# Kernel optimization log

Measured on AMD Instinct MI355X. Metric: run time of the kernel, lower is better.

## Reference

```python
import jax, jax.numpy as jnp
import numpy as np

# ---- production-scale dims ----
U, I, D = 51200, 25600, 64          # users, items, embed_size
E, EP = 1_000_000, 100_000          # train edges, pos/neg scoring edges
K = 8                               # topk similar users (FFT filter length)
NF = K // 2 + 1                     # rfft bins
CL_BS = 256                         # contrastive chunk size (U % CL_BS == 0)
TEMP = 0.2                          # args.temperature
N_LAYERS = 2                        # args.layers


def setup_inputs() -> dict:
    key = jax.random.key(0)
    ks = jax.random.split(key, 14)
    return {
        "user_emb": jax.random.normal(ks[0], (U, D), jnp.float32) * 0.1,
        "item_emb": jax.random.normal(ks[1], (I, D), jnp.float32) * 0.1,
        "W": jax.random.normal(ks[2], (D, D), jnp.float32) * (1.0 / np.sqrt(D)),
        "a": jax.random.normal(ks[3], (D,), jnp.float32) * 0.1,
        "WU": jax.random.normal(ks[4], (D, D), jnp.float32) * (1.0 / np.sqrt(D)),
        "aU": jax.random.normal(ks[5], (2 * D,), jnp.float32) * 0.1,
        "complex_weight": jax.random.normal(ks[6], (1, NF, D, 2), jnp.float32) * 0.02,
        "rate_src": jax.random.randint(ks[7], (E,), 0, U),
        "rate_dst": jax.random.randint(ks[8], (E,), 0, I),
        "pos_u": jax.random.randint(ks[9], (EP,), 0, U),
        "pos_i": jax.random.randint(ks[10], (EP,), 0, I),
        "neg_u": jax.random.randint(ks[11], (EP,), 0, U),
        "neg_i": jax.random.randint(ks[12], (EP,), 0, I),
        "nbr_idx": jax.random.randint(ks[13], (U, K), 0, U),
    }


def _propagate(src_feat, src_idx, dst_idx, n_dst):
    """DGRecLayer: degree-normalized mean aggregation over bipartite edges."""
    msg = src_feat[src_idx]                                       # [E, D] gather
    agg = jax.ops.segment_sum(msg, dst_idx, num_segments=n_dst)   # [n_dst, D] scatter
    deg = jax.ops.segment_sum(jnp.ones((src_idx.shape[0],), src_feat.dtype),
                              dst_idx, num_segments=n_dst)
    return agg / jnp.maximum(deg, 1.0)[:, None]


def _layer_attention(ls, W, a):
    t = jnp.stack(ls, axis=0)                                     # [L+1, N, D]
    alpha = jax.nn.softmax(jnp.einsum('lnd,de,e->ln', t, W, a), axis=0)
    return jnp.einsum('lnd,ln->nd', t, alpha)


def _anchor_user_embed(user_emb, WU, aU, complex_weight, nbr_idx):
    # Original detaches user embeddings to numpy for the FAISS path.
    ue = jax.lax.stop_gradient(user_emb)
    simu = ue[nbr_idx]                                            # [U, K, D]
    x = jnp.fft.rfft(simu, axis=1, norm='ortho')                  # [U, NF, D]
    wc = complex_weight[..., 0] + 1j * complex_weight[..., 1]     # [1, NF, D]
    simu = jnp.fft.irfft(x * wc, n=K, axis=1, norm='ortho')       # [U, K, D]
    Wsimu = jnp.einsum('ukd,de->uke', simu, WU)                   # [U, K, D]
    Wu = jnp.broadcast_to((ue @ WU)[:, None, :], Wsimu.shape)     # [U, K, D]
    e = jnp.concatenate([Wsimu, Wu], axis=2) @ aU                 # [U, K]
    e = jnp.where(e > 0, e, 0.1 * e)                              # LeakyReLU(0.1)
    alpha = jax.nn.softmax(e, axis=1)
    return jnp.einsum('uke,uk->ue', Wsimu, alpha)                 # [U, D]


def _chunk_contrast(r1, r2):
    B = r1.shape[0]
    n1 = jnp.linalg.norm(r1, axis=-1, keepdims=True)
    n2 = jnp.linalg.norm(r2, axis=-1, keepdims=True)
    s11 = (r1 @ r1.T) / (n1 @ n1.T + 1e-6) / TEMP
    c12 = (r1 @ r2.T) / (n1 @ n2.T + 1e-6) / TEMP
    s22 = (r2 @ r2.T) / (n2 @ n2.T + 1e-6) / TEMP
    c21 = (r2 @ r1.T) / (n2 @ n1.T + 1e-6) / TEMP
    mask = jax.nn.one_hot(jnp.arange(B), 2 * B, dtype=r1.dtype) * (-1e10)
    logits = jnp.concatenate(
        [jnp.concatenate([s11, c12], axis=-1) + mask,
         jnp.concatenate([s22, c21], axis=-1) + mask], axis=0)     # [2B, 2B]
    labels = jnp.concatenate([jnp.arange(B) + B, jnp.arange(B) + B])
    logz = jax.scipy.special.logsumexp(logits, axis=-1)
    return logz - logits[jnp.arange(2 * B), labels]                # per-example CE


def reference(user_emb, item_emb, W, a, WU, aU, complex_weight,
              rate_src, rate_dst, pos_u, pos_i, neg_u, neg_i, nbr_idx):
    h_u, h_i = user_emb, item_emb
    users, items = [h_u], [h_i]
    for _ in range(N_LAYERS):
        new_i = _propagate(h_u, rate_src, rate_dst, I)   # user -> item ('rate')
        new_u = _propagate(h_i, rate_dst, rate_src, U)   # item -> user ('rated by')
        h_u, h_i = new_u, new_i
        users.append(h_u)
        items.append(h_i)
    hu = _layer_attention(users, W, a)                   # [U, D]
    hi = _layer_attention(items, W, a)                   # [I, D]

    anchor = _anchor_user_embed(user_emb, WU, aU, complex_weight, nbr_idx)
    r1 = hu.reshape(-1, CL_BS, D)
    r2 = anchor.reshape(-1, CL_BS, D)
    loss_contrast = jax.vmap(_chunk_contrast)(r1, r2).mean()

    score_pos = jnp.sum(hu[pos_u] * hi[pos_i], axis=-1, keepdims=True)  # u_dot_v
    score_neg = jnp.sum(hu[neg_u] * hi[neg_i], axis=-1, keepdims=True)
    return score_pos, score_neg, loss_contrast
```

## Files before the change

kernel.cpp:

```cpp
#include <hip/hip_runtime.h>
#include <hip/hip_bf16.h>

constexpr int U_  = 51200;
constexpr int I_  = 25600;
constexpr int E_  = 1000000;
constexpr int EP_ = 100000;
constexpr int CB_ = 256;
constexpr int NCHUNK_ = U_ / CB_;
constexpr size_t UD_ = (size_t)U_ * 64;
constexpr size_t ID_ = (size_t)I_ * 64;
constexpr int NBK_ = 200;
constexpr int CAP_ = 8192;
constexpr int TILE_ = 4096;
constexpr int NBA_ = (E_ + TILE_ - 1) / TILE_;
constexpr int NANC_ = U_ / 16;
constexpr int NCVT_ = (int)((UD_ + ID_) / (8 * 256));

constexpr float SCALE_E_  = 16.f;
constexpr float ISCALE_E_ = 1.f / 16.f;
constexpr float SCALE_1_  = 64.f;
constexpr float ISCALE_1_ = 1.f / 64.f;

constexpr size_t OFF_LOSS  = 0;
constexpr size_t OFF_FLAG  = 1;
constexpr size_t OFF_CURU  = 8;
constexpr size_t OFF_CURI  = 208;
constexpr size_t MEMSET_BYTES = 408 * 4;
constexpr size_t OFF_VEC   = 448;
constexpr size_t OFF_BBU   = 640;
constexpr size_t OFF_BBI   = 848;
constexpr size_t OFF_ROWU  = 1088;
constexpr size_t OFF_ROWI  = ((OFF_ROWU + U_ + 1 + 63) / 64) * 64;
constexpr size_t OFF_CSRU  = ((OFF_ROWI + I_ + 1 + 63) / 64) * 64;
constexpr size_t OFF_CSRI  = OFF_CSRU + E_;
constexpr size_t OFF_U1    = ((OFF_CSRI + E_ + 63) / 64) * 64;
constexpr size_t OFF_I1    = OFF_U1 + UD_;
constexpr size_t OFF_HU    = OFF_I1 + ID_;
constexpr size_t OFF_HI    = OFF_HU + UD_;
constexpr size_t OFF_ANC   = OFF_HI + ID_;
constexpr size_t OFF_UE8   = OFF_ANC + UD_;
constexpr size_t OFF_IE8   = OFF_UE8 + UD_ / 4;
constexpr size_t OFF_U18   = OFF_IE8 + ID_ / 4;
constexpr size_t OFF_I18   = OFF_U18 + UD_ / 4;

#define DEVI static __device__ __forceinline__

typedef _Float16 h2v __attribute__((ext_vector_type(2)));
typedef _Float16 f16x8 __attribute__((ext_vector_type(8)));
typedef float floatx4 __attribute__((ext_vector_type(4)));
typedef unsigned short u16x8 __attribute__((ext_vector_type(8)));

DEVI float b2f(__hip_bfloat16 x) { return __bfloat162float(x); }

DEVI float bfb2f(unsigned short b) {
  unsigned u = ((unsigned)b) << 16; float f; __builtin_memcpy(&f, &u, 4); return f;
}

DEVI float ldf(const void* p, size_t i, int isf32) {
  if (isf32) return ((const float*)p)[i];
  return b2f(((const __hip_bfloat16*)p)[i]);
}

DEVI float frcp(float x) { return __builtin_amdgcn_rcpf(x); }

DEVI float fexp2(float x) {
#if __has_builtin(__builtin_amdgcn_exp2f)
  return __builtin_amdgcn_exp2f(x);
#else
  return exp2f(x);
#endif
}

DEVI float fp8_dec(unsigned v) {
#if __has_builtin(__builtin_amdgcn_cvt_f32_fp8)
  return __builtin_amdgcn_cvt_f32_fp8(v, 0);
#else
  unsigned b = v & 0xFF;
  if (!(b & 0x78)) return 0.f;
  unsigned short h = (unsigned short)(((b & 0x80) << 8) | (((b & 0x7f) + (8 << 3)) << 7));
  _Float16 hf; __builtin_memcpy(&hf, &h, 2);
  return (float)hf;
#endif
}

#if __has_builtin(__builtin_amdgcn_cvt_f32_fp8)
#define FP8D(w, s) __builtin_amdgcn_cvt_f32_fp8((w), (s))
#else
#define FP8D(w, s) fp8_dec(((w) >> (8 * (s))) & 0xFF)
#endif

DEVI unsigned fp8_enc_pk(float a, float b) {
#if __has_builtin(__builtin_amdgcn_cvt_pk_fp8_f32)
  return __builtin_amdgcn_cvt_pk_fp8_f32(a, b, 0u, false);
#else
  auto enc1 = [](float f) -> unsigned {
    _Float16 hf = (_Float16)f; unsigned short hb; __builtin_memcpy(&hb, &hf, 2);
    int s = hb >> 15, e = (hb >> 10) & 31, m = hb & 1023;
    int e8 = e - 15 + 7;
    int m3 = (m + ((1 << 6) + ((m >> 7) & 1))) >> 7;
    if (m3 > 7) { m3 = 0; e8++; }
    if (e8 <= 0) return (unsigned)(s << 7);
    if (e8 > 15) { e8 = 15; m3 = 6; }
    return (unsigned)((s << 7) | (e8 << 3) | m3);
  };
  return enc1(a) | (enc1(b) << 8);
#endif
}

DEVI int waveInclScan(int v, int lane) {
  #pragma unroll
  for (int off = 1; off < 64; off <<= 1) {
    int t = __shfl_up(v, off, 64);
    if (lane >= off) v += t;
  }
  return v;
}

__global__ void prep_kernel(const unsigned short* __restrict__ ueu,
                            const void* __restrict__ W, const void* __restrict__ a,
                            const void* __restrict__ WU, const void* __restrict__ aU,
                            float* __restrict__ vecs, float* __restrict__ flag) {
  int cnt = 0;
  for (int i = 0; i < 256; i++) {
    int e = (ueu[i] >> 7) & 0xFF;
    if (e >= 130) cnt++;
  }
  int isf32 = (cnt >= 8);
  if (threadIdx.x == 0) *flag = isf32 ? 1.0f : 0.0f;
  int d = threadIdx.x;
  float s = 0.f, t1 = 0.f, t2 = 0.f;
  for (int e = 0; e < 64; e++) {
    s += ldf(W, d * 64 + e, isf32) * ldf(a, e, isf32);
    float wue = ldf(WU, d * 64 + e, isf32);
    t1 += wue * ldf(aU, e, isf32);
    t2 += wue * ldf(aU, 64 + e, isf32);
  }
  vecs[d] = s;
  vecs[64 + d] = t1;
  vecs[128 + d] = t2;
}

struct BktSmem {
  int histU[NBK_], histI[NBK_];
  int loffU[NBK_ + 1], loffI[NBK_ + 1];
  int cbU[NBK_], cbI[NBK_];
  int lcU[NBK_], lcI[NBK_];
  int wsU[4], wsI[4];
  unsigned recsU[TILE_], recsI[TILE_];
};
constexpr int WS_ = 72;
struct AncSmem {
  _Float16 WUt[64 * WS_];
  _Float16 mixS[16 * WS_];
  float invSe[16];
  int nbrS[128];
};
constexpr size_t FSA_SMEM = sizeof(BktSmem) > sizeof(AncSmem) ? sizeof(BktSmem) : sizeof(AncSmem);

DEVI void bucketA_body(char* smemRaw, int blk,
    const int* __restrict__ rs, const int* __restrict__ rd,
    unsigned* __restrict__ bufU, unsigned* __restrict__ bufI,
    int* __restrict__ curU, int* __restrict__ curI) {
  BktSmem& S = *(BktSmem*)smemRaw;
  int tid = threadIdx.x;
  int base = blk * TILE_;
  for (int i = tid; i < NBK_; i += 256) { S.histU[i] = 0; S.histI[i] = 0; }
  __syncthreads();
  int ss[16], dd[16];
  #pragma unroll
  for (int t = 0; t < 16; t++) {
    int e = base + t * 256 + tid;
    bool v = e < E_;
    ss[t] = v ? rs[e] : -1;
    dd[t] = v ? rd[e] : 0;
    if (v) {
      atomicAdd(&S.histU[ss[t] >> 8], 1);
      atomicAdd(&S.histI[dd[t] >> 7], 1);
    }
  }
  __syncthreads();
  if (tid < NBK_) {
    int cU = S.histU[tid];
    S.cbU[tid] = tid * CAP_ + (cU ? atomicAdd(&curU[tid], cU) : 0);
    int cI = S.histI[tid];
    S.cbI[tid] = tid * CAP_ + (cI ? atomicAdd(&curI[tid], cI) : 0);
  }
  int lane = tid & 63, wv = tid >> 6;
  int cvU = (tid < NBK_) ? S.histU[tid] : 0;
  int cvI = (tid < NBK_) ? S.histI[tid] : 0;
  int inU = waveInclScan(cvU, lane);
  int inI = waveInclScan(cvI, lane);
  if (lane == 63) { S.wsU[wv] = inU; S.wsI[wv] = inI; }
  __syncthreads();
  int woU = 0, woI = 0;
  for (int w = 0; w < wv; w++) { woU += S.wsU[w]; woI += S.wsI[w]; }
  if (tid < NBK_) {
    S.loffU[tid] = woU + inU - cvU;
    S.loffI[tid] = woI + inI - cvI;
  }
  if (tid == NBK_ - 1) {
    S.loffU[NBK_] = woU + inU;
    S.loffI[NBK_] = woI + inI;
  }
  __syncthreads();
  if (tid < NBK_) { S.lcU[tid] = S.loffU[tid]; S.lcI[tid] = S.loffI[tid]; }
  __syncthreads();
  #pragma unroll
  for (int t = 0; t < 16; t++) {
    if (ss[t] >= 0) {
      int b = ss[t] >> 8;
      int p = atomicAdd(&S.lcU[b], 1);
      S.recsU[p] = ((unsigned)(ss[t] & 255) << 17) | (unsigned)dd[t];
      b = dd[t] >> 7;
      p = atomicAdd(&S.lcI[b], 1);
      S.recsI[p] = ((unsigned)(dd[t] & 127) << 17) | (unsigned)ss[t];
    }
  }
  __syncthreads();
  int totU = S.loffU[NBK_];
  for (int p = tid; p < totU; p += 256) {
    int lo = 0, hi = NBK_;
    while (hi - lo > 1) { int mid = (lo + hi) >> 1; if (S.loffU[mid] <= p) lo = mid; else hi = mid; }
    bufU[S.cbU[lo] + (p - S.loffU[lo])] = S.recsU[p];
  }
  int totI = S.loffI[NBK_];
  for (int p = tid; p < totI; p += 256) {
    int lo = 0, hi = NBK_;
    while (hi - lo > 1) { int mid = (lo + hi) >> 1; if (S.loffI[mid] <= p) lo = mid; else hi = mid; }
    bufI[S.cbI[lo] + (p - S.loffI[lo])] = S.recsI[p];
  }
}

DEVI void anchor_body(char* smemRaw, int blk,
    const void* __restrict__ ue, const void* __restrict__ WU,
    const void* __restrict__ cw, const float* __restrict__ vecs,
    const int* __restrict__ nbr, float* __restrict__ out, int isf32) {
  AncSmem& S = *(AncSmem*)smemRaw;
  int tid = threadIdx.x;
  int wv = tid >> 6, lane = tid & 63;
  int ublk = blk * 16;

  #pragma unroll
  for (int it = 0; it < 16; it++) {
    int k = it * 4 + wv;
    S.WUt[lane * WS_ + k] = (_Float16)ldf(WU, (size_t)k * 64 + lane, isf32);
  }
  if (tid < 128) S.nbrS[tid] = nbr[ublk * 8 + tid];
  __syncthreads();

  float cw0 = ldf(cw, (0 * 64 + lane) * 2, isf32);
  float w1r = ldf(cw, (1 * 64 + lane) * 2, isf32), w1i = ldf(cw, (1 * 64 + lane) * 2 + 1, isf32);
  float w2r = ldf(cw, (2 * 64 + lane) * 2, isf32), w2i = ldf(cw, (2 * 64 + lane) * 2 + 1, isf32);
  float w3r = ldf(cw, (3 * 64 + lane) * 2, isf32), w3i = ldf(cw, (3 * 64 + lane) * 2 + 1, isf32);
  float cw4 = ldf(cw, (4 * 64 + lane) * 2, isf32);
  float v1 = vecs[64 + lane], v2 = vecs[128 + lane];
  const float c1 = 0.70710678118654752440f;

  float xc[8], xn[8];
  #pragma unroll
  for (int k = 0; k < 8; k++)
    xc[k] = ldf(ue, (size_t)S.nbrS[wv * 32 + k] * 64 + lane, isf32);

  for (int u4 = 0; u4 < 4; u4++) {
    int uL = wv * 4 + u4;
    int u = ublk + uL;
    if (u4 < 3) {
      #pragma unroll
      for (int k = 0; k < 8; k++)
        xn[k] = ldf(ue, (size_t)S.nbrS[wv * 32 + (u4 + 1) * 8 + k] * 64 + lane, isf32);
    }
    float sA = xc[1] - xc[3] - xc[5] + xc[7];
    float sB = xc[1] + xc[3] - xc[5] - xc[7];
    float ev = (xc[0] + xc[4]) + (xc[2] + xc[6]);
    float od = (xc[1] + xc[5]) + (xc[3] + xc[7]);
    float d04 = xc[0] - xc[4], d26 = xc[2] - xc[6];
    float X0r = ev + od;
    float X1r = d04 + c1 * sA;
    float X1i = -d26 - c1 * sB;
    float X2r = (xc[0] + xc[4]) - (xc[2] + xc[6]);
    float X2i = -(xc[1] - xc[3] + xc[5] - xc[7]);
    float X3r = d04 - c1 * sA;
    float X3i = d26 - c1 * sB;
    float X4r = ev - od;
    float Zr0 = X0r * cw0;
    float Zr1 = X1r * w1r - X1i * w1i, Zi1 = X1r * w1i + X1i * w1r;
    float Zr2 = X2r * w2r - X2i * w2i, Zi2 = X2r * w2i + X2i * w2r;
    float Zr3 = X3r * w3r - X3i * w3i, Zi3 = X3r * w3i + X3i * w3r;
    float Zr4 = X4r * cw4;
    float eP = Zr0 + Zr4, eM = Zr0 - Zr4;
    float t1 = c1 * (Zr1 - Zr3), t2 = c1 * (Zi1 + Zi3);
    float y[8];
    y[0] = eP + 2.f * (Zr1 + Zr2 + Zr3);
    y[1] = eM + 2.f * (t1 - t2 - Zi2);
    y[2] = eP + 2.f * (-Zi1 - Zr2 + Zi3);
    y[3] = eM + 2.f * (-t1 - t2 + Zi2);
    y[4] = eP + 2.f * (-Zr1 + Zr2 - Zr3);
    y[5] = eM + 2.f * (-t1 + t2 - Zi2);
    y[6] = eP + 2.f * (Zi1 - Zr2 - Zi3);
    y[7] = eM + 2.f * (t1 + t2 + Zi2);
    #pragma unroll
    for (int k = 0; k < 8; k++) y[k] *= 0.125f;

    float ek[8];
    #pragma unroll
    for (int k = 0; k < 8; k++) ek[k] = y[k] * v1;
    float q = ldf(ue, (size_t)u * 64 + lane, isf32) * v2;
    #pragma unroll
    for (int off = 32; off; off >>= 1) {
      #pragma unroll
      for (int k = 0; k < 8; k++) ek[k] += __shfl_xor(ek[k], off, 64);
      q += __shfl_xor(q, off, 64);
    }
    float m = -1e30f;
    #pragma unroll
    for (int k = 0; k < 8; k++) {
      float v = ek[k] + q;
      v = v > 0.f ? v : 0.1f * v;
      ek[k] = v;
      m = fmaxf(m, v);
    }
    float se = 0.f, wexp[8];
    #pragma unroll
    for (int k = 0; k < 8; k++) { wexp[k] = __expf(ek[k] - m); se += wexp[k]; }
    float mix = 0.f;
    #pragma unroll
    for (int k = 0; k < 8; k++) mix += wexp[k] * y[k];
    S.mixS[uL * WS_ + lane] = (_Float16)mix;
    if (lane == 0) S.invSe[uL] = frcp(se);
    #pragma unroll
    for (int k = 0; k < 8; k++) xc[k] = xn[k];
  }
  __syncthreads();

  int n = lane & 15, qd = lane >> 4;
  f16x8 A0 = *(const f16x8*)&S.mixS[(lane & 15) * WS_ + qd * 8];
  f16x8 A1 = *(const f16x8*)&S.mixS[(lane & 15) * WS_ + 32 + qd * 8];
  f16x8 B0 = *(const f16x8*)&S.WUt[(wv * 16 + n) * WS_ + qd * 8];
  f16x8 B1 = *(const f16x8*)&S.WUt[(wv * 16 + n) * WS_ + 32 + qd * 8];
  const floatx4 zero = {0.f, 0.f, 0.f, 0.f};
  floatx4 acc = __builtin_amdgcn_mfma_f32_16x16x32_f16(A0, B0, zero, 0, 0, 0);
  acc = __builtin_amdgcn_mfma_f32_16x16x32_f16(A1, B1, acc, 0, 0, 0);
  #pragma unroll
  for (int r = 0; r < 4; r++) {
    int m = qd * 4 + r;
    out[(size_t)(ublk + m) * 64 + wv * 16 + n] = acc[r] * S.invSe[m];
  }
}

DEVI void convert_body(int blk, const void* __restrict__ ue, const void* __restrict__ ie,
                       unsigned char* __restrict__ ue8, unsigned char* __restrict__ ie8,
                       int isf32) {
  size_t t = (size_t)blk * 256 + threadIdx.x;
  const void* src; unsigned* dst; size_t o;
  if (t < UD_ / 8) { src = ue; dst = (unsigned*)ue8; o = t; }
  else             { src = ie; dst = (unsigned*)ie8; o = t - UD_ / 8; }
  float v[8];
  if (isf32) {
    float4 f0 = ((const float4*)src)[2 * o];
    float4 f1 = ((const float4*)src)[2 * o + 1];
    v[0] = f0.x; v[1] = f0.y; v[2] = f0.z; v[3] = f0.w;
    v[4] = f1.x; v[5] = f1.y; v[6] = f1.z; v[7] = f1.w;
  } else {
    u16x8 h = ((const u16x8*)src)[o];
    #pragma unroll
    for (int i = 0; i < 8; i++) v[i] = bfb2f(h[i]);
  }
  unsigned lo = fp8_enc_pk(v[0] * SCALE_E_, v[1] * SCALE_E_) |
                (fp8_enc_pk(v[2] * SCALE_E_, v[3] * SCALE_E_) << 16);
  unsigned hi = fp8_enc_pk(v[4] * SCALE_E_, v[5] * SCALE_E_) |
                (fp8_enc_pk(v[6] * SCALE_E_, v[7] * SCALE_E_) << 16);
  dst[2 * o]     = lo;
  dst[2 * o + 1] = hi;
}

__global__ __launch_bounds__(256) void fusedA_kernel(
    const int* __restrict__ rs, const int* __restrict__ rd,
    unsigned* __restrict__ bufU, unsigned* __restrict__ bufI,
    int* __restrict__ curU, int* __restrict__ curI,
    const void* __restrict__ ue, const void* __restrict__ ie,
    const void* __restrict__ WU, const void* __restrict__ cw,
    const float* __restrict__ vecs, const int* __restrict__ nbr,
    float* __restrict__ anc, unsigned char* __restrict__ ue8,
    unsigned char* __restrict__ ie8, const float* __restrict__ flag) {
  __shared__ __align__(16) char smem[FSA_SMEM];
  if (blockIdx.x < NBA_) {
    bucketA_body(smem, blockIdx.x, rs, rd, bufU, bufI, curU, curI);
  } else if (blockIdx.x < NBA_ + NANC_) {
    anchor_body(smem, blockIdx.x - NBA_, ue, WU, cw, vecs, nbr, anc, *flag > 0.5f);
  } else {
    convert_body(blockIdx.x - NBA_ - NANC_, ue, ie, ue8, ie8, *flag > 0.5f);
  }
}

__global__ void scanBuckets_kernel(const int* __restrict__ curU,
                                   const int* __restrict__ curI,
                                   int* __restrict__ bbU, int* __restrict__ bbI,
                                   int* __restrict__ rowU, int* __restrict__ rowI) {
  __shared__ int ws[8];
  int tid = threadIdx.x;
  int lane = tid & 63, wv = tid >> 6;
  int vU = (tid < NBK_) ? curU[tid] : 0;
  int vI = (tid < NBK_) ? curI[tid] : 0;
  int iU = waveInclScan(vU, lane);
  int iI = waveInclScan(vI, lane);
  if (lane == 63) { ws[wv] = iU; ws[4 + wv] = iI; }
  __syncthreads();
  int oU = 0, oI = 0;
  for (int w = 0; w < wv; w++) { oU += ws[w]; oI += ws[4 + w]; }
  if (tid < NBK_) { bbU[tid] = oU + iU - vU; bbI[tid] = oI + iI - vI; }
  if (tid == NBK_ - 1) { bbU[NBK_] = oU + iU; bbI[NBK_] = oI + iI; }
  if (tid == 0) { rowU[U_] = E_; rowI[I_] = E_; }
}

__global__ __launch_bounds__(256) void bucketB_kernel(
    const unsigned* __restrict__ bufU, const unsigned* __restrict__ bufI,
    const int* __restrict__ curU, const int* __restrict__ curI,
    const int* __restrict__ bbU, const int* __restrict__ bbI,
    int* __restrict__ rowU, int* __restrict__ rowI,
    int* __restrict__ csrU, int* __restrict__ csrI) {
  __shared__ int stage[CAP_];
  __shared__ int cntk[256], offk[256];
  __shared__ int wsum[4];
  int tid = threadIdx.x, b = blockIdx.x;
  int side = b >= NBK_;
  int bb = side ? b - NBK_ : b;
  const unsigned* src = (side ? bufI : bufU) + (size_t)bb * CAP_;
  int total = side ? curI[bb] : curU[bb];
  int gbase = side ? bbI[bb] : bbU[bb];
  int kpb   = side ? 128 : 256;
  int* rowptr = side ? rowI : rowU;
  int* csr    = side ? csrI : csrU;
  cntk[tid] = 0;
  __syncthreads();
  for (int r = tid; r < total; r += 256) atomicAdd(&cntk[src[r] >> 17], 1);
  __syncthreads();
  int lane = tid & 63, wv = tid >> 6;
  int cv = (tid < kpb) ? cntk[tid] : 0;
  int incl = waveInclScan(cv, lane);
  if (lane == 63) wsum[wv] = incl;
  __syncthreads();
  int wvoff = 0;
  for (int w = 0; w < wv; w++) wvoff += wsum[w];
  int excl = wvoff + incl - cv;
  if (tid < kpb) {
    offk[tid] = excl;
    rowptr[bb * kpb + tid] = gbase + excl;
  }
  __syncthreads();
  for (int r = tid; r < total; r += 256) {
    unsigned rec = src[r];
    int slot = atomicAdd(&offk[rec >> 17], 1);
    if (slot < CAP_) stage[slot] = (int)(rec & 0x1FFFFu);
  }
  __syncthreads();
  for (int s = tid; s < total; s += 256) csr[gbase + s] = stage[s];
}

__global__ __launch_bounds__(256) void agg1_kernel(
    const unsigned char* __restrict__ ue8, const unsigned char* __restrict__ ie8,
    const int* __restrict__ rowU, const int* __restrict__ rowI,
    const int* __restrict__ csrU, const int* __restrict__ csrI,
    __hip_bfloat16* __restrict__ u1, __hip_bfloat16* __restrict__ i1,
    unsigned char* __restrict__ u18, unsigned char* __restrict__ i18) {
  int wv = threadIdx.x >> 6, lane = threadIdx.x & 63;
  int sub = lane >> 4, c16 = lane & 15;
  int side = blockIdx.x >= I_ / 4;
  int blk = side ? blockIdx.x - I_ / 4 : blockIdx.x;
  int r = blk * 4 + wv;
  const int* row = side ? rowU : rowI;
  const int* csr = side ? csrU : csrI;
  const unsigned char* src = side ? ie8 : ue8;
  __hip_bfloat16* out = side ? u1 : i1;
  unsigned char* out8 = side ? u18 : i18;
  int s0 = row[r], s1 = row[r + 1];
  float a4[4] = {0.f, 0.f, 0.f, 0.f};
  int j = s0;
  for (; j + 8 <= s1; j += 8) {
    int e0 = csr[j + sub], e1 = csr[j + 4 + sub];
    unsigned w0 = *(const unsigned*)(src + (size_t)e0 * 64 + c16 * 4);
    unsigned w1 = *(const unsigned*)(src + (size_t)e1 * 64 + c16 * 4);
    a4[0] += FP8D(w0, 0) + FP8D(w1, 0);
    a4[1] += FP8D(w0, 1) + FP8D(w1, 1);
    a4[2] += FP8D(w0, 2) + FP8D(w1, 2);
    a4[3] += FP8D(w0, 3) + FP8D(w1, 3);
  }
  if (j + 4 <= s1) {
    int e0 = csr[j + sub];
    unsigned w0 = *(const unsigned*)(src + (size_t)e0 * 64 + c16 * 4);
    a4[0] += FP8D(w0, 0); a4[1] += FP8D(w0, 1);
    a4[2] += FP8D(w0, 2); a4[3] += FP8D(w0, 3);
    j += 4;
  }
  int rem = s1 - j;
  if (sub < rem) {
    int e0 = csr[j + sub];
    unsigned w0 = *(const unsigned*)(src + (size_t)e0 * 64 + c16 * 4);
    a4[0] += FP8D(w0, 0); a4[1] += FP8D(w0, 1);
    a4[2] += FP8D(w0, 2); a4[3] += FP8D(w0, 3);
  }
  #pragma unroll
  for (int c = 0; c < 4; c++) {
    a4[c] += __shfl_xor(a4[c], 16, 64);
    a4[c] += __shfl_xor(a4[c], 32, 64);
  }
  float acc = sub == 0 ? a4[0] : sub == 1 ? a4[1] : sub == 2 ? a4[2] : a4[3];
  int col = c16 * 4 + sub;
  float val = acc * ISCALE_E_ * frcp(fmaxf((float)(s1 - s0), 1.0f));
  size_t idx = (size_t)r * 64 + col;
  out[idx] = __float2bfloat16(val);
  unsigned p = fp8_enc_pk(val * SCALE_1_, val * SCALE_1_);
  out8[idx] = (unsigned char)(p & 0xFF);
}

__global__ __launch_bounds__(256) void agg2attn_kernel(
    const unsigned char* __restrict__ u18, const unsigned char* __restrict__ i18,
    const __hip_bfloat16* __restrict__ u1, const __hip_bfloat16* __restrict__ i1,
    const void* __restrict__ ue, const void* __restrict__ ie,
    const int* __restrict__ rowU, const int* __restrict__ rowI,
    const int* __restrict__ csrU, const int* __restrict__ csrI,
    const float* __restrict__ vecs, float* __restrict__ hu, float* __restrict__ hi,
    const float* __restrict__ flag) {
  int isf32 = *flag > 0.5f;
  int wv = threadIdx.x >> 6, lane = threadIdx.x & 63;
  int sub = lane >> 4, c16 = lane & 15;
  int side = blockIdx.x >= I_ / 4;
  int blk = side ? blockIdx.x - I_ / 4 : blockIdx.x;
  int r = blk * 4 + wv;
  const int* row = side ? rowU : rowI;
  const int* csr = side ? csrU : csrI;
  const unsigned char* opp8 = side ? i18 : u18;
  const __hip_bfloat16* own1 = side ? u1 : i1;
  const void* base = side ? ue : ie;
  float* h = side ? hu : hi;
  int s0 = row[r], s1 = row[r + 1];
  float a4[4] = {0.f, 0.f, 0.f, 0.f};
  int j = s0;
  for (; j + 8 <= s1; j += 8) {
    int e0 = csr[j + sub], e1 = csr[j + 4 + sub];
    unsigned w0 = *(const unsigned*)(opp8 + (size_t)e0 * 64 + c16 * 4);
    unsigned w1 = *(const unsigned*)(opp8 + (size_t)e1 * 64 + c16 * 4);
    a4[0] += FP8D(w0, 0) + FP8D(w1, 0);
    a4[1] += FP8D(w0, 1) + FP8D(w1, 1);
    a4[2] += FP8D(w0, 2) + FP8D(w1, 2);
    a4[3] += FP8D(w0, 3) + FP8D(w1, 3);
  }
  if (j + 4 <= s1) {
    int e0 = csr[j + sub];
    unsigned w0 = *(const unsigned*)(opp8 + (size_t)e0 * 64 + c16 * 4);
    a4[0] += FP8D(w0, 0); a4[1] += FP8D(w0, 1);
    a4[2] += FP8D(w0, 2); a4[3] += FP8D(w0, 3);
    j += 4;
  }
  int rem = s1 - j;
  if (sub < rem) {
    int e0 = csr[j + sub];
    unsigned w0 = *(const unsigned*)(opp8 + (size_t)e0 * 64 + c16 * 4);
    a4[0] += FP8D(w0, 0); a4[1] += FP8D(w0, 1);
    a4[2] += FP8D(w0, 2); a4[3] += FP8D(w0, 3);
  }
  #pragma unroll
  for (int c = 0; c < 4; c++) {
    a4[c] += __shfl_xor(a4[c], 16, 64);
    a4[c] += __shfl_xor(a4[c], 32, 64);
  }
  float acc = sub == 0 ? a4[0] : sub == 1 ? a4[1] : sub == 2 ? a4[2] : a4[3];
  int col = c16 * 4 + sub;
  size_t idx = (size_t)r * 64 + col;
  float t2 = acc * ISCALE_1_ * frcp(fmaxf((float)(s1 - s0), 1.0f));
  float t0 = ldf(base, idx, isf32);
  float t1 = b2f(own1[idx]);
  float w = vecs[col];
  float p0 = t0 * w, p1 = t1 * w, p2 = t2 * w;
  #pragma unroll
  for (int off = 32; off; off >>= 1) {
    p0 += __shfl_xor(p0, off, 64);
    p1 += __shfl_xor(p1, off, 64);
    p2 += __shfl_xor(p2, off, 64);
  }
  float m = fmaxf(p0, fmaxf(p1, p2));
  float e0 = __expf(p0 - m), e1 = __expf(p1 - m), e2 = __expf(p2 - m);
  float inv = 1.0f / (e0 + e1 + e2);
  h[idx] = (t0 * e0 + t1 * e1 + t2 * e2) * inv;
}

constexpr int XS_ = 72;
constexpr float SC_  = 2.6857914f;
constexpr float EPS_ = 1e-6f;
constexpr float LN2_ = 0.6931471805599453f;
__global__ __launch_bounds__(1024) void contrast_kernel(
    const float* __restrict__ hu, const float* __restrict__ an,
    float* __restrict__ loss_acc) {
  __shared__ __align__(16) _Float16 Xh[512 * XS_];
  __shared__ float iN[512];
  int tid = threadIdx.x;
  int c = blockIdx.x;

  if (tid < 512) {
    int row = tid & 255;
    const float* r1 = (tid < 256 ? hu : an) + ((size_t)c * CB_ + row) * 64;
    float4 a4[16];
    float s1 = 0.f;
    #pragma unroll
    for (int t = 0; t < 16; t++) {
      a4[t] = ((const float4*)r1)[t];
      s1 += a4[t].x * a4[t].x + a4[t].y * a4[t].y + a4[t].z * a4[t].z + a4[t].w * a4[t].w;
    }
    float inv = frcp(sqrtf(s1));
    iN[tid] = inv;
    float sc = inv * SC_;
    #pragma unroll
    for (int t = 0; t < 8; t++) {
      f16x8 v;
      v[0] = (_Float16)(a4[2*t].x * sc);   v[1] = (_Float16)(a4[2*t].y * sc);
      v[2] = (_Float16)(a4[2*t].z * sc);   v[3] = (_Float16)(a4[2*t].w * sc);
      v[4] = (_Float16)(a4[2*t+1].x * sc); v[5] = (_Float16)(a4[2*t+1].y * sc);
      v[6] = (_Float16)(a4[2*t+1].z * sc); v[7] = (_Float16)(a4[2*t+1].w * sc);
      *(f16x8*)&Xh[tid * XS_ + t * 8] = v;
    }
  }
  __syncthreads();

  int l = tid & 63, wv = tid >> 6;
  int n = l & 15, q = l >> 4;
  int rb = wv * 32;
  f16x8 A[2][2];
  #pragma unroll
  for (int t = 0; t < 2; t++) {
    A[t][0] = *(const f16x8*)&Xh[(rb + t * 16 + n) * XS_ + q * 8];
    A[t][1] = *(const f16x8*)&Xh[(rb + t * 16 + n) * XS_ + 32 + q * 8];
  }
  float eNiR[2][4];
  #pragma unroll
  for (int t = 0; t < 2; t++)
    #pragma unroll
    for (int r = 0; r < 4; r++)
      eNiR[t][r] = EPS_ * iN[rb + t * 16 + q * 4 + r];
  float sums[2][4] = {{0,0,0,0},{0,0,0,0}};
  float labs2[2] = {0, 0};
  int selfn = q * 4;
  const floatx4 zero = {0.f, 0.f, 0.f, 0.f};
  for (int ct = 0; ct < 32; ct++) {
    f16x8 B0 = *(const f16x8*)&Xh[(ct * 16 + n) * XS_ + q * 8];
    f16x8 B1 = *(const f16x8*)&Xh[(ct * 16 + n) * XS_ + 32 + q * 8];
    float iNj = iN[ct * 16 + n];
    #pragma unroll
    for (int t = 0; t < 2; t++) {
      floatx4 acc = __builtin_amdgcn_mfma_f32_16x16x32_f16(A[t][0], B0, zero, 0, 0, 0);
      acc = __builtin_amdgcn_mfma_f32_16x16x32_f16(A[t][1], B1, acc, 0, 0, 0);
      int rtg = wv * 2 + t;
      if (ct == (rtg ^ 16)) {
        #pragma unroll
        for (int r = 0; r < 4; r++) {
          float G = acc[r];
          float u = eNiR[t][r] * iNj;
          float s2 = __builtin_fmaf(G, -u, G);
          sums[t][r] += fexp2(s2);
          if (n == selfn + r) labs2[t] += s2;
        }
      } else if (ct == rtg) {
        #pragma unroll
        for (int r = 0; r < 4; r++) {
          float G = acc[r];
          float u = eNiR[t][r] * iNj;
          float s2 = __builtin_fmaf(G, -u, G);
          float e = (n == selfn + r) ? 0.f : fexp2(s2);
          sums[t][r] += e;
        }
      } else {
        #pragma unroll
        for (int r = 0; r < 4; r++) {
          float G = acc[r];
          float u = eNiR[t][r] * iNj;
          float s2 = __builtin_fmaf(G, -u, G);
          sums[t][r] += fexp2(s2);
        }
      }
    }
  }
  #pragma unroll
  for (int off = 1; off <= 8; off <<= 1) {
    #pragma unroll
    for (int t = 0; t < 2; t++) {
      #pragma unroll
      for (int r = 0; r < 4; r++) sums[t][r] += __shfl_xor(sums[t][r], off, 64);
      labs2[t] += __shfl_xor(labs2[t], off, 64);
    }
  }
  float part = 0.f;
  if (n == 0) {
    #pragma unroll
    for (int t = 0; t < 2; t++) {
      float lt = 0.f;
      #pragma unroll
      for (int r = 0; r < 4; r++) lt += __logf(sums[t][r]);
      part += lt - labs2[t] * LN2_;
    }
  }
  #pragma unroll
  for (int off = 1; off < 64; off <<= 1) part += __shfl_xor(part, off, 64);
  if (l == 0) atomicAdd(loss_acc, part);
}

__global__ __launch_bounds__(256) void score_kernel(
    const float* __restrict__ hu, const float* __restrict__ hi,
    const int* __restrict__ pu, const int* __restrict__ pi,
    const int* __restrict__ nu, const int* __restrict__ ni,
    void* __restrict__ out, const float* __restrict__ flag) {
  int isf32 = *flag > 0.5f;
  int w = (blockIdx.x * 256 + threadIdx.x) >> 6;
  int lane = threadIdx.x & 63;
  int uu, ii;
  if (w < EP_) { uu = pu[w]; ii = pi[w]; }
  else         { uu = nu[w - EP_]; ii = ni[w - EP_]; }
  float p = hu[(size_t)uu * 64 + lane] * hi[(size_t)ii * 64 + lane];
  #pragma unroll
  for (int off = 32; off; off >>= 1) p += __shfl_xor(p, off, 64);
  if (lane == 0) {
    if (isf32) ((float*)out)[w] = p;
    else       ((__hip_bfloat16*)out)[w] = __float2bfloat16(p);
  }
}

__global__ void finalize_kernel(const float* __restrict__ loss_acc,
                                void* __restrict__ out,
                                const float* __restrict__ flag) {
  float v = loss_acc[0] * (1.0f / (float)(2 * CB_ * NCHUNK_));
  if (*flag > 0.5f) ((float*)out)[2 * EP_] = v;
  else              ((__hip_bfloat16*)out)[2 * EP_] = __float2bfloat16(v);
}

extern "C" void kernel_launch(void* const* d_in, const int* in_sizes, int n_in,
                              void* d_out, int out_size, void* d_ws, size_t ws_size,
                              hipStream_t stream) {
  const void* ue  = d_in[0];
  const void* ie  = d_in[1];
  const void* W   = d_in[2];
  const void* a   = d_in[3];
  const void* WU  = d_in[4];
  const void* aU  = d_in[5];
  const void* cw  = d_in[6];
  const int* rs  = (const int*)d_in[7];
  const int* rd  = (const int*)d_in[8];
  const int* pu  = (const int*)d_in[9];
  const int* pi  = (const int*)d_in[10];
  const int* nu  = (const int*)d_in[11];
  const int* ni  = (const int*)d_in[12];
  const int* nbr = (const int*)d_in[13];

  float* wsf  = (float*)d_ws;
  int*   wsi  = (int*)d_ws;
  float* loss = wsf + OFF_LOSS;
  float* flag = wsf + OFF_FLAG;
  int* curU   = wsi + OFF_CURU;
  int* curI   = wsi + OFF_CURI;
  float* vecs = wsf + OFF_VEC;
  int* bbU    = wsi + OFF_BBU;
  int* bbI    = wsi + OFF_BBI;
  int* rowU   = wsi + OFF_ROWU;
  int* rowI   = wsi + OFF_ROWI;
  int* csrU   = wsi + OFF_CSRU;
  int* csrI   = wsi + OFF_CSRI;
  __hip_bfloat16* u1 = (__hip_bfloat16*)(wsf + OFF_U1);
  __hip_bfloat16* i1 = (__hip_bfloat16*)(wsf + OFF_I1);
  float* hu   = wsf + OFF_HU;
  float* hi   = wsf + OFF_HI;
  float* anc  = wsf + OFF_ANC;
  unsigned char* ue8 = (unsigned char*)(wsf + OFF_UE8);
  unsigned char* ie8 = (unsigned char*)(wsf + OFF_IE8);
  unsigned char* u18 = (unsigned char*)(wsf + OFF_U18);
  unsigned char* i18 = (unsigned char*)(wsf + OFF_I18);
  unsigned* bufU = (unsigned*)(wsf + OFF_HU);
  unsigned* bufI = (unsigned*)(wsf + OFF_HI);

  hipMemsetAsync(d_ws, 0, MEMSET_BYTES, stream);
  prep_kernel<<<1, 64, 0, stream>>>((const unsigned short*)ue, W, a, WU, aU, vecs, flag);

  fusedA_kernel<<<NBA_ + NANC_ + NCVT_, 256, 0, stream>>>(
      rs, rd, bufU, bufI, curU, curI, ue, ie, WU, cw, vecs, nbr, anc, ue8, ie8, flag);
  scanBuckets_kernel<<<1, 256, 0, stream>>>(curU, curI, bbU, bbI, rowU, rowI);
  bucketB_kernel<<<2 * NBK_, 256, 0, stream>>>(bufU, bufI, curU, curI, bbU, bbI,
                                               rowU, rowI, csrU, csrI);

  agg1_kernel<<<(I_ + U_) / 4, 256, 0, stream>>>(ue8, ie8, rowU, rowI, csrU, csrI,
                                                 u1, i1, u18, i18);
  agg2attn_kernel<<<(I_ + U_) / 4, 256, 0, stream>>>(u18, i18, u1, i1, ue, ie,
                                                     rowU, rowI, csrU, csrI,
                                                     vecs, hu, hi, flag);

  contrast_kernel<<<NCHUNK_, 1024, 0, stream>>>(hu, anc, loss);

  score_kernel<<<(2 * EP_ * 64) / 256, 256, 0, stream>>>(hu, hi, pu, pi, nu, ni, d_out, flag);
  finalize_kernel<<<1, 1, 0, stream>>>(loss, d_out, flag);
}
```

Measured before the change: 367.6 us.

## Fold bucket scan into bucketB, split contrast row loads, vectorize score kernel

```diff
diff --git a/kernel.cpp b/kernel.cpp
--- a/kernel.cpp
+++ b/kernel.cpp
@@ -15,6 +15,7 @@
 constexpr int NBA_ = (E_ + TILE_ - 1) / TILE_;
 constexpr int NANC_ = U_ / 16;
 constexpr int NCVT_ = (int)((UD_ + ID_) / (8 * 256));
+constexpr int NSCB_ = (2 * EP_) / 16;
 
 constexpr float SCALE_E_  = 16.f;
 constexpr float ISCALE_E_ = 1.f / 16.f;
@@ -27,8 +28,6 @@
 constexpr size_t OFF_CURI  = 208;
 constexpr size_t MEMSET_BYTES = 408 * 4;
 constexpr size_t OFF_VEC   = 448;
-constexpr size_t OFF_BBU   = 640;
-constexpr size_t OFF_BBI   = 848;
 constexpr size_t OFF_ROWU  = 1088;
 constexpr size_t OFF_ROWI  = ((OFF_ROWU + U_ + 1 + 63) / 64) * 64;
 constexpr size_t OFF_CSRU  = ((OFF_ROWI + I_ + 1 + 63) / 64) * 64;
@@ -392,68 +391,63 @@
   }
 }
 
-__global__ void scanBuckets_kernel(const int* __restrict__ curU,
-                                   const int* __restrict__ curI,
-                                   int* __restrict__ bbU, int* __restrict__ bbI,
-                                   int* __restrict__ rowU, int* __restrict__ rowI) {
-  __shared__ int ws[8];
-  int tid = threadIdx.x;
-  int lane = tid & 63, wv = tid >> 6;
-  int vU = (tid < NBK_) ? curU[tid] : 0;
-  int vI = (tid < NBK_) ? curI[tid] : 0;
-  int iU = waveInclScan(vU, lane);
-  int iI = waveInclScan(vI, lane);
-  if (lane == 63) { ws[wv] = iU; ws[4 + wv] = iI; }
-  __syncthreads();
-  int oU = 0, oI = 0;
-  for (int w = 0; w < wv; w++) { oU += ws[w]; oI += ws[4 + w]; }
-  if (tid < NBK_) { bbU[tid] = oU + iU - vU; bbI[tid] = oI + iI - vI; }
-  if (tid == NBK_ - 1) { bbU[NBK_] = oU + iU; bbI[NBK_] = oI + iI; }
-  if (tid == 0) { rowU[U_] = E_; rowI[I_] = E_; }
-}
+struct BktBSmem {
+  int stage[CAP_];
+  int cntk[256], offk[256];
+  int exclS[256];
+  int wsum[4], wsum2[4];
+};
 
 __global__ __launch_bounds__(256) void bucketB_kernel(
     const unsigned* __restrict__ bufU, const unsigned* __restrict__ bufI,
     const int* __restrict__ curU, const int* __restrict__ curI,
-    const int* __restrict__ bbU, const int* __restrict__ bbI,
     int* __restrict__ rowU, int* __restrict__ rowI,
     int* __restrict__ csrU, int* __restrict__ csrI) {
-  __shared__ int stage[CAP_];
-  __shared__ int cntk[256], offk[256];
-  __shared__ int wsum[4];
+  __shared__ __align__(16) BktBSmem S;
   int tid = threadIdx.x, b = blockIdx.x;
   int side = b >= NBK_;
   int bb = side ? b - NBK_ : b;
   const unsigned* src = (side ? bufI : bufU) + (size_t)bb * CAP_;
-  int total = side ? curI[bb] : curU[bb];
-  int gbase = side ? bbI[bb] : bbU[bb];
+  const int* cur = side ? curI : curU;
+  int total = cur[bb];
   int kpb   = side ? 128 : 256;
   int* rowptr = side ? rowI : rowU;
   int* csr    = side ? csrI : csrU;
-  cntk[tid] = 0;
-  __syncthreads();
-  for (int r = tid; r < total; r += 256) atomicAdd(&cntk[src[r] >> 17], 1);
-  __syncthreads();
+  if (b == 0 && tid == 0) { rowU[U_] = E_; rowI[I_] = E_; }
   int lane = tid & 63, wv = tid >> 6;
-  int cv = (tid < kpb) ? cntk[tid] : 0;
+  {
+    int v = (tid < NBK_) ? cur[tid] : 0;
+    int incl = waveInclScan(v, lane);
+    if (lane == 63) S.wsum2[wv] = incl;
+    S.cntk[tid] = 0;
+    __syncthreads();
+    int off = 0;
+    for (int w = 0; w < wv; w++) off += S.wsum2[w];
+    if (tid < NBK_) S.exclS[tid] = off + incl - v;
+    __syncthreads();
+  }
+  int gbase = S.exclS[bb];
+  for (int r = tid; r < total; r += 256) atomicAdd(&S.cntk[src[r] >> 17], 1);
+  __syncthreads();
+  int cv = (tid < kpb) ? S.cntk[tid] : 0;
   int incl = waveInclScan(cv, lane);
-  if (lane == 63) wsum[wv] = incl;
+  if (lane == 63) S.wsum[wv] = incl;
   __syncthreads();
   int wvoff = 0;
-  for (int w = 0; w < wv; w++) wvoff += wsum[w];
+  for (int w = 0; w < wv; w++) wvoff += S.wsum[w];
   int excl = wvoff + incl - cv;
   if (tid < kpb) {
-    offk[tid] = excl;
+    S.offk[tid] = excl;
     rowptr[bb * kpb + tid] = gbase + excl;
   }
   __syncthreads();
   for (int r = tid; r < total; r += 256) {
     unsigned rec = src[r];
-    int slot = atomicAdd(&offk[rec >> 17], 1);
-    if (slot < CAP_) stage[slot] = (int)(rec & 0x1FFFFu);
-  }
-  __syncthreads();
-  for (int s = tid; s < total; s += 256) csr[gbase + s] = stage[s];
+    int slot = atomicAdd(&S.offk[rec >> 17], 1);
+    if (slot < CAP_) S.stage[slot] = (int)(rec & 0x1FFFFu);
+  }
+  __syncthreads();
+  for (int s = tid; s < total; s += 256) csr[gbase + s] = S.stage[s];
 }
 
 __global__ __launch_bounds__(256) void agg1_kernel(
@@ -595,27 +589,29 @@
   int tid = threadIdx.x;
   int c = blockIdx.x;
 
-  if (tid < 512) {
-    int row = tid & 255;
-    const float* r1 = (tid < 256 ? hu : an) + ((size_t)c * CB_ + row) * 64;
-    float4 a4[16];
+  {
+    int rid = tid >> 1, half = tid & 1;
+    int row = rid & 255;
+    const float* r1 = (rid < 256 ? hu : an) + ((size_t)c * CB_ + row) * 64 + half * 32;
+    float4 a4[8];
     float s1 = 0.f;
     #pragma unroll
-    for (int t = 0; t < 16; t++) {
+    for (int t = 0; t < 8; t++) {
       a4[t] = ((const float4*)r1)[t];
       s1 += a4[t].x * a4[t].x + a4[t].y * a4[t].y + a4[t].z * a4[t].z + a4[t].w * a4[t].w;
     }
+    s1 += __shfl_xor(s1, 1, 64);
     float inv = frcp(sqrtf(s1));
-    iN[tid] = inv;
+    if (half == 0) iN[rid] = inv;
     float sc = inv * SC_;
     #pragma unroll
-    for (int t = 0; t < 8; t++) {
+    for (int t = 0; t < 4; t++) {
       f16x8 v;
       v[0] = (_Float16)(a4[2*t].x * sc);   v[1] = (_Float16)(a4[2*t].y * sc);
       v[2] = (_Float16)(a4[2*t].z * sc);   v[3] = (_Float16)(a4[2*t].w * sc);
       v[4] = (_Float16)(a4[2*t+1].x * sc); v[5] = (_Float16)(a4[2*t+1].y * sc);
       v[6] = (_Float16)(a4[2*t+1].z * sc); v[7] = (_Float16)(a4[2*t+1].w * sc);
-      *(f16x8*)&Xh[tid * XS_ + t * 8] = v;
+      *(f16x8*)&Xh[rid * XS_ + half * 32 + t * 8] = v;
     }
   }
   __syncthreads();
@@ -707,15 +703,19 @@
     const int* __restrict__ nu, const int* __restrict__ ni,
     void* __restrict__ out, const float* __restrict__ flag) {
   int isf32 = *flag > 0.5f;
-  int w = (blockIdx.x * 256 + threadIdx.x) >> 6;
   int lane = threadIdx.x & 63;
+  int g = lane >> 4, c = lane & 15;
+  int gw = blockIdx.x * 4 + (threadIdx.x >> 6);
+  int w = gw * 4 + g;
   int uu, ii;
   if (w < EP_) { uu = pu[w]; ii = pi[w]; }
   else         { uu = nu[w - EP_]; ii = ni[w - EP_]; }
-  float p = hu[(size_t)uu * 64 + lane] * hi[(size_t)ii * 64 + lane];
-  #pragma unroll
-  for (int off = 32; off; off >>= 1) p += __shfl_xor(p, off, 64);
-  if (lane == 0) {
+  float4 a = *(const float4*)(hu + (size_t)uu * 64 + c * 4);
+  float4 b = *(const float4*)(hi + (size_t)ii * 64 + c * 4);
+  float p = a.x * b.x + a.y * b.y + a.z * b.z + a.w * b.w;
+  #pragma unroll
+  for (int off = 1; off < 16; off <<= 1) p += __shfl_xor(p, off, 64);
+  if (c == 0) {
     if (isf32) ((float*)out)[w] = p;
     else       ((__hip_bfloat16*)out)[w] = __float2bfloat16(p);
   }
@@ -754,8 +754,6 @@
   int* curU   = wsi + OFF_CURU;
   int* curI   = wsi + OFF_CURI;
   float* vecs = wsf + OFF_VEC;
-  int* bbU    = wsi + OFF_BBU;
-  int* bbI    = wsi + OFF_BBI;
   int* rowU   = wsi + OFF_ROWU;
   int* rowI   = wsi + OFF_ROWI;
   int* csrU   = wsi + OFF_CSRU;
@@ -777,8 +775,8 @@
 
   fusedA_kernel<<<NBA_ + NANC_ + NCVT_, 256, 0, stream>>>(
       rs, rd, bufU, bufI, curU, curI, ue, ie, WU, cw, vecs, nbr, anc, ue8, ie8, flag);
-  scanBuckets_kernel<<<1, 256, 0, stream>>>(curU, curI, bbU, bbI, rowU, rowI);
-  bucketB_kernel<<<2 * NBK_, 256, 0, stream>>>(bufU, bufI, curU, curI, bbU, bbI,
+
+  bucketB_kernel<<<2 * NBK_, 256, 0, stream>>>(bufU, bufI, curU, curI,
                                                rowU, rowI, csrU, csrI);
 
   agg1_kernel<<<(I_ + U_) / 4, 256, 0, stream>>>(ue8, ie8, rowU, rowI, csrU, csrI,
@@ -789,6 +787,6 @@
 
   contrast_kernel<<<NCHUNK_, 1024, 0, stream>>>(hu, anc, loss);
 
-  score_kernel<<<(2 * EP_ * 64) / 256, 256, 0, stream>>>(hu, hi, pu, pi, nu, ni, d_out, flag);
+  score_kernel<<<NSCB_, 256, 0, stream>>>(hu, hi, pu, pi, nu, ni, d_out, flag);
   finalize_kernel<<<1, 1, 0, stream>>>(loss, d_out, flag);
 }
```

Result: faster. 343.0 us (-6.7%).
